# Optimization experiments

Measured on AMD Instinct MI355X. Metric: run time of the kernel, lower is better.

Reference implementation:

```python
import jax, jax.numpy as jnp
import numpy as np

N, H, E, R, Q = 10000, 128, 160000, 32, 1
CUT = 5.0  # cutoff_upper, cutoff_lower = 0


def setup_inputs() -> dict:
    key = jax.random.key(0)
    ks = jax.random.split(key, 16)

    def w(k, shape, fan_in):
        return jax.random.normal(k, shape, jnp.float32) / np.sqrt(fan_in).astype(np.float32)

    return dict(
        X=jax.random.normal(ks[0], (N, H, 3, 3), jnp.float32),
        charges=jax.random.normal(ks[1], (N, Q), jnp.float32),
        edge_attr=jax.random.normal(ks[2], (E, R), jnp.float32),
        edge_weight=jax.random.uniform(ks[3], (E,), jnp.float32, 0.0, CUT),
        W1=w(ks[4], (H, R + 2 * Q), R + 2 * Q), b1=jnp.zeros((H,), jnp.float32),
        W2=w(ks[5], (2 * H, H), H), b2=jnp.zeros((2 * H,), jnp.float32),
        W3=w(ks[6], (3 * H, 2 * H), 2 * H), b3=jnp.zeros((3 * H,), jnp.float32),
        Wt0=w(ks[7], (H, H), H), Wt1=w(ks[8], (H, H), H), Wt2=w(ks[9], (H, H), H),
        Wt3=w(ks[10], (H, H), H), Wt4=w(ks[11], (H, H), H), Wt5=w(ks[12], (H, H), H),
        edge_index=jax.random.randint(ks[13], (2, E), 0, N),
    )


def tensor_norm(T):
    return jnp.sum(T * T, axis=(-2, -1))  # [N, H]


def decompose(T):
    # I: mean of diagonal (scalar per channel); A: skew part; S: traceless symmetric part
    I = jnp.trace(T, axis1=-2, axis2=-1) / 3.0  # [N, H]
    Tt = jnp.swapaxes(T, -2, -1)
    A = 0.5 * (T - Tt)
    S = 0.5 * (T + Tt) - I[..., None, None] * jnp.eye(3, dtype=T.dtype)
    return I, A, S


def chlin(T, W):
    # channel-mixing linear on [N, H, 3, 3]; torch Linear: y_o = sum_h x_h W[o, h]
    return jnp.einsum('nhij,oh->noij', T, W)


def vec_to_skew(v):
    # v: [N, H, 3] -> skew-symmetric [N, H, 3, 3]
    z = jnp.zeros_like(v[..., 0])
    return jnp.stack([
        jnp.stack([z, -v[..., 2], v[..., 1]], -1),
        jnp.stack([v[..., 2], z, -v[..., 0]], -1),
        jnp.stack([-v[..., 1], v[..., 0], z], -1),
    ], -2)


def skew_to_vec(A):
    return jnp.stack([A[..., 2, 1], A[..., 0, 2], A[..., 1, 0]], -1)


def reference(X, charges, edge_attr, edge_weight, W1, b1, W2, b2, W3, b3,
              Wt0, Wt1, Wt2, Wt3, Wt4, Wt5, edge_index):
    eye = jnp.eye(3, dtype=X.dtype)
    src, dst = edge_index[0], edge_index[1]
    n = X.shape[0]

    # cosine cutoff (cutoff_lower = 0)
    C = 0.5 * (jnp.cos(jnp.pi * edge_weight / CUT) + 1.0) * (edge_weight < CUT)

    # edge scalar MLP
    x = jnp.concatenate([edge_attr, charges[src], charges[dst]], axis=-1)
    x = jax.nn.silu(x @ W1.T + b1)
    x = jax.nn.silu(x @ W2.T + b2)
    x = jax.nn.silu(x @ W3.T + b3)
    x = (x * C[:, None]).reshape(-1, 3, H)  # [E, 3, H]

    X = X / (tensor_norm(X) + 1.0)[..., None, None]
    I, A, S = decompose(X)
    I = I @ Wt0.T
    A = chlin(A, Wt1)
    S = chlin(S, Wt2)
    Y = A + S + I[..., None, None] * eye

    # message passing: gather at dst, weight by edge scalars, scatter-add to src
    Im = jax.ops.segment_sum(x[:, 0, :] * I[dst], src, num_segments=n)
    Am = jax.ops.segment_sum(x[:, 1, :, None] * skew_to_vec(A)[dst], src, num_segments=n)
    Sm = jax.ops.segment_sum(x[:, 2, :, None, None] * S[dst], src, num_segments=n)
    msg = vec_to_skew(Am) + Sm + Im[..., None, None] * eye

    # O(3) equivariance: symmetrized product
    M = jnp.matmul(msg, Y) + jnp.matmul(Y, msg)
    I, A, S = decompose(M)

    _X = A + S + I[..., None, None] * eye
    normp1 = tensor_norm(_X) + 1.0
    I = I / normp1
    A = A / normp1[..., None, None]
    S = S / normp1[..., None, None]
    I = I @ Wt3.T
    A = chlin(A, Wt4)
    S = chlin(S, Wt5)
    dX = A + S + I[..., None, None] * eye
    return X + dX + jnp.matmul(dX, dX)
```

## Files before the change

### kernel.cpp

```cpp
#include <hip/hip_runtime.h>

#define NN  10000
#define HD  128
#define EE  160000
#define RD  32
#define NH  (NN * HD)

typedef __attribute__((ext_vector_type(8))) short short8_t;
typedef __attribute__((ext_vector_type(4))) float f32x4_t;
typedef __attribute__((ext_vector_type(4))) int   int4_t;

__device__ __forceinline__ float silu_f(float z) {
    return z * __builtin_amdgcn_rcpf(1.0f + __expf(-z));
}
__device__ __forceinline__ short f2b(float v) {
    unsigned u = __float_as_uint(v);
    unsigned r = (u + 0x7FFFu + ((u >> 16) & 1u)) >> 16;
    return (short)r;
}
__device__ __forceinline__ float b2f(short s) {
    return __uint_as_float(((unsigned)(unsigned short)s) << 16);
}
__device__ __forceinline__ unsigned cvt_pk(float a, float b) {
    unsigned r;
    asm("v_cvt_pk_bf16_f32 %0, %1, %2" : "=v"(r) : "v"(a), "v"(b));
    return r;
}

__global__ __launch_bounds__(256) void k_wconv(
    const float* __restrict__ W1, const float* __restrict__ W2,
    const float* __restrict__ W3,
    const float* __restrict__ Wt0, const float* __restrict__ Wt1,
    const float* __restrict__ Wt2, const float* __restrict__ Wt3,
    const float* __restrict__ Wt4, const float* __restrict__ Wt5,
    short* __restrict__ W1b, short* __restrict__ W2b, short* __restrict__ W3b,
    short* __restrict__ WtPh, short* __restrict__ WtPl,
    short* __restrict__ WtFh, short* __restrict__ WtFl)
{
    const int i = blockIdx.x * 256 + threadIdx.x;
    if (i < 8192) {
        const int j = i & 7, lane = (i >> 3) & 63;
        const int kb = (i >> 9) & 1, ct = i >> 10;
        const int n = ct * 16 + (lane & 15);
        const int k = kb * 32 + (lane >> 4) * 8 + j;
        W1b[i] = (k < 34) ? f2b(W1[n * 34 + k]) : (short)0;
        return;
    }
    int j2 = i - 8192;
    if (j2 < 32768) {
        const int j = j2 & 7, lane = (j2 >> 3) & 63;
        const int kb = (j2 >> 9) & 3, ct = j2 >> 11;
        const int n = ct * 16 + (lane & 15);
        const int k = kb * 32 + (lane >> 4) * 8 + j;
        W2b[j2] = f2b(W2[n * 128 + k]);
        return;
    }
    j2 -= 32768;
    if (j2 < 98304) {
        const int j = j2 & 7, lane = (j2 >> 3) & 63;
        const int kb = (j2 >> 9) & 7, ct = j2 >> 12;
        const int n = ct * 16 + (lane & 15);
        const int k = kb * 32 + (lane >> 4) * 8 + j;
        W3b[j2] = f2b(W3[n * 256 + k]);
        return;
    }
    j2 -= 98304;
    if (j2 < 6 * 16384) {
        const int m = j2 >> 14, idx = j2 & 16383;
        const float* src = (m == 0) ? Wt0 : (m == 1) ? Wt1 : (m == 2) ? Wt2
                         : (m == 3) ? Wt3 : (m == 4) ? Wt4 : Wt5;
        const float w = src[idx];
        const short hi = f2b(w);
        const short lo = f2b(w - b2f(hi));
        if (m < 3) { WtPh[m * 16384 + idx] = hi; WtPl[m * 16384 + idx] = lo; }
        else       { WtFh[(m - 3) * 16384 + idx] = hi; WtFl[(m - 3) * 16384 + idx] = lo; }
    }
}


template <bool YBF16>
__global__ __launch_bounds__(512, 4) void k_mix_prep(
    const float* __restrict__ X,
    const short* __restrict__ Wh, const short* __restrict__ Wl,
    float* __restrict__ Yf, short* __restrict__ ybf)
{
    extern __shared__ __align__(16) char smem[];
    short* sBh = (short*)smem;
    short* sBl = sBh + 144 * 128;
    float* sC  = (float*)smem;

    const int tid = threadIdx.x;
    const int n0  = blockIdx.x * 16;

#pragma unroll 2
    for (int i = 0; i < 4; i++) {
        const int p  = i * 512 + tid;
        const int nl = p >> 7, h = p & 127;
        const float* t = X + ((size_t)((n0 + nl) * HD + h)) * 9;
        float T[9];
#pragma unroll
        for (int q = 0; q < 9; q++) T[q] = t[q];
        float nrm = 0.f;
#pragma unroll
        for (int q = 0; q < 9; q++) nrm = fmaf(T[q], T[q], nrm);
        const float inv = 1.0f / (nrm + 1.0f);
#pragma unroll
        for (int q = 0; q < 9; q++) T[q] *= inv;
        const float I = (T[0] + T[4] + T[8]) * (1.0f / 3.0f);
        float dec[9];
        dec[0] = I;
        dec[1] = 0.5f * (T[7] - T[5]);
        dec[2] = 0.5f * (T[2] - T[6]);
        dec[3] = 0.5f * (T[3] - T[1]);
        dec[4] = T[0] - I;
        dec[5] = 0.5f * (T[1] + T[3]);
        dec[6] = 0.5f * (T[2] + T[6]);
        dec[7] = T[4] - I;
        dec[8] = 0.5f * (T[5] + T[7]);
        const int sw = (nl & 7) << 3;
        const int hx = h ^ sw;
#pragma unroll
        for (int c = 0; c < 9; c++) {
            const float v  = dec[c];
            const short hi = f2b(v);
            const short lo = f2b(v - b2f(hi));
            const int idx = (c * 16 + nl) * 128 + hx;
            sBh[idx] = hi;
            sBl[idx] = lo;
        }
    }
    __syncthreads();

    const int lane = tid & 63, wid = tid >> 6;
    const int l15 = lane & 15, g = lane >> 4;
    f32x4_t acc[9];
#pragma unroll
    for (int c = 0; c < 9; c++) acc[c] = {0.f, 0.f, 0.f, 0.f};

    const int bsw = (l15 & 7) << 3;
    const int o   = wid * 16 + l15;
#pragma unroll
    for (int k = 0; k < 4; k++) {
        const int k0  = k * 32 + g * 8;
        const int ksw = k0 ^ bsw;
#pragma unroll
        for (int w = 0; w < 3; w++) {
            const size_t aoff = (size_t)w * 16384 + (size_t)o * 128 + k0;
            const short8_t Ah = *(const short8_t*)(Wh + aoff);
            const short8_t Al = *(const short8_t*)(Wl + aoff);
            const int ct0 = (w == 0) ? 0 : (w == 1 ? 1 : 4);
            const int ctn = (w == 0) ? 1 : (w == 1 ? 3 : 5);
            for (int cc = 0; cc < ctn; cc++) {
                const int ct = ct0 + cc;
                const int boff = (ct * 16 + l15) * 128 + ksw;
                const short8_t Bh = *(const short8_t*)&sBh[boff];
                const short8_t Bl = *(const short8_t*)&sBl[boff];
                acc[ct] = __builtin_amdgcn_mfma_f32_16x16x32_bf16(Al, Bh, acc[ct], 0, 0, 0);
                acc[ct] = __builtin_amdgcn_mfma_f32_16x16x32_bf16(Ah, Bl, acc[ct], 0, 0, 0);
                acc[ct] = __builtin_amdgcn_mfma_f32_16x16x32_bf16(Ah, Bh, acc[ct], 0, 0, 0);
            }
        }
    }
    __syncthreads();

    const int csw = (l15 & 7) << 2;
    {
        const int o0 = wid * 16 + g * 4;
#pragma unroll
        for (int ct = 0; ct < 9; ct++)
            *(f32x4_t*)&sC[(ct * 16 + l15) * 128 + (o0 ^ csw)] = acc[ct];
    }
    __syncthreads();

    for (int i = tid; i < 144 * 32; i += 512) {
        const int row = i >> 5, q = i & 31;
        const int c = row >> 4, nl = row & 15;
        const int sw = (nl & 7) << 2;
        const f32x4_t v = *(const f32x4_t*)&sC[row * 128 + ((q * 4) ^ sw)];
        const size_t oo = (size_t)c * NH + (size_t)(n0 + nl) * HD + q * 4;
        if constexpr (YBF16) {
            uint2 u;
            u.x = cvt_pk(v[0], v[1]);
            u.y = cvt_pk(v[2], v[3]);
            *(uint2*)&ybf[oo] = u;
        } else {
            *(f32x4_t*)&Yf[oo] = v;
        }
    }
}

template <bool FUSED>
__global__ __launch_bounds__(512, 4) void k_mix_fin(
    const float* __restrict__ X,
    const float* __restrict__ Yf,  const float* __restrict__ MSGf,
    const short* __restrict__ Ybf, const short* __restrict__ XC,
    const int* __restrict__ offs,  const int* __restrict__ DSTS,
    const short* __restrict__ Wh,  const short* __restrict__ Wl,
    float* __restrict__ outp)
{
    extern __shared__ __align__(16) char smem[];
    short* sBh = (short*)smem;
    short* sBl = sBh + 144 * 128;
    float* sC  = (float*)smem;

    const int tid = threadIdx.x;
    const int n0  = blockIdx.x * 16;

    for (int i = 0; i < 4; i++) {
        const int p  = i * 512 + tid;
        const int nl = p >> 7, h = p & 127;
        const int basep = (n0 + nl) * HD + h;
        float yv[9], mv[9];
        if constexpr (FUSED) {
            const int n = n0 + nl;
            const int beg = offs[n], end = offs[n + 1];
#pragma unroll
            for (int c = 0; c < 9; c++) mv[c] = 0.f;
            for (int pp = beg; pp < end; ++pp) {
                const int dst = DSTS[pp];
                const size_t xb = (size_t)pp * 384;
                const float x0 = b2f(XC[xb + h]);
                const float x1 = b2f(XC[xb + 128 + h]);
                const float x2 = b2f(XC[xb + 256 + h]);
                const int yb = dst * HD + h;
                mv[0] = fmaf(x0, b2f(Ybf[0 * (size_t)NH + yb]), mv[0]);
                mv[1] = fmaf(x1, b2f(Ybf[1 * (size_t)NH + yb]), mv[1]);
                mv[2] = fmaf(x1, b2f(Ybf[2 * (size_t)NH + yb]), mv[2]);
                mv[3] = fmaf(x1, b2f(Ybf[3 * (size_t)NH + yb]), mv[3]);
                mv[4] = fmaf(x2, b2f(Ybf[4 * (size_t)NH + yb]), mv[4]);
                mv[5] = fmaf(x2, b2f(Ybf[5 * (size_t)NH + yb]), mv[5]);
                mv[6] = fmaf(x2, b2f(Ybf[6 * (size_t)NH + yb]), mv[6]);
                mv[7] = fmaf(x2, b2f(Ybf[7 * (size_t)NH + yb]), mv[7]);
                mv[8] = fmaf(x2, b2f(Ybf[8 * (size_t)NH + yb]), mv[8]);
            }
#pragma unroll
            for (int c = 0; c < 9; c++) yv[c] = b2f(Ybf[(size_t)c * NH + basep]);
        } else {
#pragma unroll
            for (int c = 0; c < 9; c++) {
                yv[c] = Yf[(size_t)c * NH + basep];
                mv[c] = MSGf[(size_t)c * NH + basep];
            }
        }
        float Yt[9], G[9];
        {
            const float I = yv[0], a0 = yv[1], a1 = yv[2], a2 = yv[3];
            const float s00 = yv[4], s01 = yv[5], s02 = yv[6], s11 = yv[7], s12 = yv[8];
            const float s22 = -s00 - s11;
            Yt[0] = I + s00; Yt[1] = s01 - a2; Yt[2] = s02 + a1;
            Yt[3] = s01 + a2; Yt[4] = I + s11; Yt[5] = s12 - a0;
            Yt[6] = s02 - a1; Yt[7] = s12 + a0; Yt[8] = I + s22;
        }
        {
            const float I = mv[0], a0 = mv[1], a1 = mv[2], a2 = mv[3];
            const float s00 = mv[4], s01 = mv[5], s02 = mv[6], s11 = mv[7], s12 = mv[8];
            const float s22 = -s00 - s11;
            G[0] = I + s00; G[1] = s01 - a2; G[2] = s02 + a1;
            G[3] = s01 + a2; G[4] = I + s11; G[5] = s12 - a0;
            G[6] = s02 - a1; G[7] = s12 + a0; G[8] = I + s22;
        }
        float M[9];
#pragma unroll
        for (int r = 0; r < 3; r++)
#pragma unroll
            for (int cc = 0; cc < 3; cc++) {
                float a = 0.f;
#pragma unroll
                for (int k = 0; k < 3; k++)
                    a += G[r * 3 + k] * Yt[k * 3 + cc]
                       + Yt[r * 3 + k] * G[k * 3 + cc];
                M[r * 3 + cc] = a;
            }
        const float I2 = (M[0] + M[4] + M[8]) * (1.0f / 3.0f);
        const float a0 = 0.5f * (M[7] - M[5]);
        const float a1 = 0.5f * (M[2] - M[6]);
        const float a2 = 0.5f * (M[3] - M[1]);
        const float s00 = M[0] - I2, s11 = M[4] - I2;
        const float s01 = 0.5f * (M[1] + M[3]);
        const float s02 = 0.5f * (M[2] + M[6]);
        const float s12 = 0.5f * (M[5] + M[7]);
        const float s22 = -s00 - s11;
        const float nrm = 2.f * (a0 * a0 + a1 * a1 + a2 * a2)
                        + (s00 * s00 + s11 * s11 + s22 * s22)
                        + 2.f * (s01 * s01 + s02 * s02 + s12 * s12)
                        + 3.f * I2 * I2;
        const float inv = 1.0f / (nrm + 1.0f);
        float dec[9];
        dec[0] = I2 * inv;  dec[1] = a0 * inv;  dec[2] = a1 * inv;
        dec[3] = a2 * inv;  dec[4] = s00 * inv; dec[5] = s01 * inv;
        dec[6] = s02 * inv; dec[7] = s11 * inv; dec[8] = s12 * inv;

        const int sw = (nl & 7) << 3;
        const int hx = h ^ sw;
#pragma unroll
        for (int c = 0; c < 9; c++) {
            const float v  = dec[c];
            const short hi = f2b(v);
            const short lo = f2b(v - b2f(hi));
            const int idx = (c * 16 + nl) * 128 + hx;
            sBh[idx] = hi;
            sBl[idx] = lo;
        }
    }
    __syncthreads();

    const int lane = tid & 63, wid = tid >> 6;
    const int l15 = lane & 15, g = lane >> 4;
    f32x4_t acc[9];
#pragma unroll
    for (int c = 0; c < 9; c++) acc[c] = {0.f, 0.f, 0.f, 0.f};

    const int bsw = (l15 & 7) << 3;
    const int o   = wid * 16 + l15;
#pragma unroll
    for (int k = 0; k < 4; k++) {
        const int k0  = k * 32 + g * 8;
        const int ksw = k0 ^ bsw;
#pragma unroll
        for (int w = 0; w < 3; w++) {
            const size_t aoff = (size_t)w * 16384 + (size_t)o * 128 + k0;
            const short8_t Ah = *(const short8_t*)(Wh + aoff);
            const short8_t Al = *(const short8_t*)(Wl + aoff);
            const int ct0 = (w == 0) ? 0 : (w == 1 ? 1 : 4);
            const int ctn = (w == 0) ? 1 : (w == 1 ? 3 : 5);
            for (int cc = 0; cc < ctn; cc++) {
                const int ct = ct0 + cc;
                const int boff = (ct * 16 + l15) * 128 + ksw;
                const short8_t Bh = *(const short8_t*)&sBh[boff];
                const short8_t Bl = *(const short8_t*)&sBl[boff];
                acc[ct] = __builtin_amdgcn_mfma_f32_16x16x32_bf16(Al, Bh, acc[ct], 0, 0, 0);
                acc[ct] = __builtin_amdgcn_mfma_f32_16x16x32_bf16(Ah, Bl, acc[ct], 0, 0, 0);
                acc[ct] = __builtin_amdgcn_mfma_f32_16x16x32_bf16(Ah, Bh, acc[ct], 0, 0, 0);
            }
        }
    }
    __syncthreads();

    const int csw = (l15 & 7) << 2;
    {
        const int o0 = wid * 16 + g * 4;
#pragma unroll
        for (int ct = 0; ct < 9; ct++)
            *(f32x4_t*)&sC[(ct * 16 + l15) * 128 + (o0 ^ csw)] = acc[ct];
    }
    __syncthreads();

#pragma unroll 2
    for (int i = 0; i < 4; i++) {
        const int p  = i * 512 + tid;
        const int nl = p >> 7, oo = p & 127;
        const int sw = (nl & 7) << 2;
        const int ox = oo ^ sw;
        float a9[9];
#pragma unroll
        for (int c = 0; c < 9; c++) a9[c] = sC[(c * 16 + nl) * 128 + ox];
        float D[9];
        {
            const float I = a9[0], a0 = a9[1], a1 = a9[2], a2 = a9[3];
            const float s00 = a9[4], s01 = a9[5], s02 = a9[6];
            const float s11 = a9[7], s12 = a9[8];
            const float s22 = -s00 - s11;
            D[0] = I + s00; D[1] = s01 - a2; D[2] = s02 + a1;
            D[3] = s01 + a2; D[4] = I + s11; D[5] = s12 - a0;
            D[6] = s02 - a1; D[7] = s12 + a0; D[8] = I + s22;
        }
        const size_t xbase = ((size_t)((n0 + nl) * HD + oo)) * 9;
        float T[9];
#pragma unroll
        for (int q = 0; q < 9; q++) T[q] = X[xbase + q];
        float nrm = 0.f;
#pragma unroll
        for (int q = 0; q < 9; q++) nrm = fmaf(T[q], T[q], nrm);
        const float inv = 1.0f / (nrm + 1.0f);
        float* op = outp + xbase;
#pragma unroll
        for (int r = 0; r < 3; r++)
#pragma unroll
            for (int cc = 0; cc < 3; cc++) {
                float dd2 = 0.f;
#pragma unroll
                for (int k = 0; k < 3; k++)
                    dd2 = fmaf(D[r * 3 + k], D[k * 3 + cc], dd2);
                op[r * 3 + cc] = T[r * 3 + cc] * inv + D[r * 3 + cc] + dd2;
            }
    }
}

__global__ __launch_bounds__(256) void k_count(const int* __restrict__ EI,
                                               int* __restrict__ cnt)
{
    const int e = blockIdx.x * 256 + threadIdx.x;
    atomicAdd(&cnt[EI[e]], 1);
}

__global__ __launch_bounds__(256) void k_scan(const int* __restrict__ cnt,
                                              int* __restrict__ offs,
                                              int* __restrict__ cur)
{
    __shared__ int part[256];
    const int tid = threadIdx.x;
    const int per = (NN + 255) / 256;
    int s = 0;
    for (int i = 0; i < per; i++) {
        const int idx = tid * per + i;
        if (idx < NN) s += cnt[idx];
    }
    part[tid] = s;
    __syncthreads();
    if (tid == 0) {
        int r = 0;
        for (int i = 0; i < 256; i++) { const int t = part[i]; part[i] = r; r += t; }
        offs[NN] = r;
    }
    __syncthreads();
    int run = part[tid];
    for (int i = 0; i < per; i++) {
        const int idx = tid * per + i;
        if (idx < NN) {
            offs[idx] = run;
            cur[idx]  = run;
            run += cnt[idx];
        }
    }
}

__global__ __launch_bounds__(256) void k_fill(const int* __restrict__ EI,
                                              int* __restrict__ cur,
                                              int* __restrict__ EIDS,
                                              int* __restrict__ DSTS)
{
    const int e = blockIdx.x * 256 + threadIdx.x;
    const int s = EI[e];
    const int pos = atomicAdd(&cur[s], 1);
    EIDS[pos] = e;
    DSTS[pos] = EI[EE + e];
}

__global__ __launch_bounds__(512, 4) void k_edge_mfma(
    const float* __restrict__ EA, const float* __restrict__ CH,
    const float* __restrict__ EW, const int*   __restrict__ EI,
    const int*   __restrict__ EIDS,
    const short* __restrict__ W1b, const float* __restrict__ b1,
    const short* __restrict__ W2b, const float* __restrict__ b2,
    const short* __restrict__ W3b, const float* __restrict__ b3,
    short* __restrict__ XC)
{
    __shared__ __align__(16) short sH2[64 * 256];
    __shared__ __align__(16) short sH1[64 * 128];
    __shared__ float sCut[64];
    __shared__ int   sEid[64];

    short* sIn = sH2;
    const int tid = threadIdx.x;
    const int e0  = blockIdx.x * 64;

    {
        int4_t z = {0, 0, 0, 0};
        ((int4_t*)sIn)[tid] = z;
        if (tid < 64) sEid[tid] = EIDS[e0 + tid];
    }
    __syncthreads();
    {
        const int ee  = tid >> 3;
        const int eid = sEid[ee];
        const float4 v = *(const float4*)(EA + (size_t)eid * RD + (tid & 7) * 4);
        const int k = (tid & 7) * 4;
        short4 sv;
        sv.x = f2b(v.x); sv.y = f2b(v.y); sv.z = f2b(v.z); sv.w = f2b(v.w);
        *(short4*)&sIn[ee * 64 + (k ^ ((ee & 7) << 3))] = sv;
        if (tid < 64) {
            const int e2  = tid;
            const int eid2 = sEid[e2];
            const int s = EI[eid2];
            const int d = EI[EE + eid2];
            const int sw = (e2 & 7) << 3;
            sIn[e2 * 64 + (32 ^ sw)] = f2b(CH[s]);
            sIn[e2 * 64 + (33 ^ sw)] = f2b(CH[d]);
            const float w = EW[eid2];
            sCut[e2] = (w < 5.0f)
                     ? 0.5f * (__cosf(0.62831853071795864769f * w) + 1.0f) : 0.0f;
        }
    }
    __syncthreads();

    const int lane = tid & 63;
    const int wid  = tid >> 6;
    const int l15  = lane & 15;
    const int g    = lane >> 4;
    const int fsw  = l15 << 3;

    {
        short8_t E1[4][2];
#pragma unroll
        for (int at = 0; at < 4; at++) {
            const int row = at * 16 + l15;
            const int x = (row & 7) << 3;
            E1[at][0] = *(const short8_t*)&sIn[row * 64 + ((g * 8) ^ x)];
            E1[at][1] = *(const short8_t*)&sIn[row * 64 + ((32 + g * 8) ^ x)];
        }
        const int ct = wid;
        const float4 b4 = *(const float4*)&b1[ct * 16 + g * 4];
        const short8_t av0 = *(const short8_t*)(W1b + (size_t)((ct * 2 + 0) * 64 + lane) * 8);
        const short8_t av1 = *(const short8_t*)(W1b + (size_t)((ct * 2 + 1) * 64 + lane) * 8);
        const int fcol = ct * 16 + g * 4;
#pragma unroll
        for (int at = 0; at < 4; at++) {
            f32x4_t acc = {b4.x, b4.y, b4.z, b4.w};
            acc = __builtin_amdgcn_mfma_f32_16x16x32_bf16(av0, E1[at][0], acc, 0, 0, 0);
            acc = __builtin_amdgcn_mfma_f32_16x16x32_bf16(av1, E1[at][1], acc, 0, 0, 0);
            const int edge = at * 16 + l15;
            uint2 u;
            u.x = cvt_pk(silu_f(acc[0]), silu_f(acc[1]));
            u.y = cvt_pk(silu_f(acc[2]), silu_f(acc[3]));
            *(uint2*)&sH1[edge * 128 + (fcol ^ fsw)] = u;
        }
    }
    __syncthreads();

    {
        short8_t E2[4][4];
#pragma unroll
        for (int at = 0; at < 4; at++) {
            const int row = at * 16 + l15;
            const int x = (row & 15) << 3;
#pragma unroll
            for (int kb = 0; kb < 4; kb++)
                E2[at][kb] = *(const short8_t*)&sH1[row * 128 + ((kb * 32 + g * 8) ^ x)];
        }
#pragma unroll
        for (int c = 0; c < 2; c++) {
            const int ct = c * 8 + wid;
            const float4 b4 = *(const float4*)&b2[ct * 16 + g * 4];
            const int fcol = ct * 16 + g * 4;
            f32x4_t acc[4];
#pragma unroll
            for (int at = 0; at < 4; at++) acc[at] = {b4.x, b4.y, b4.z, b4.w};
#pragma unroll
            for (int kb = 0; kb < 4; kb++) {
                const short8_t av = *(const short8_t*)(W2b + (size_t)((ct * 4 + kb) * 64 + lane) * 8);
#pragma unroll
                for (int at = 0; at < 4; at++)
                    acc[at] = __builtin_amdgcn_mfma_f32_16x16x32_bf16(av, E2[at][kb], acc[at], 0, 0, 0);
            }
#pragma unroll
            for (int at = 0; at < 4; at++) {
                const int edge = at * 16 + l15;
                uint2 u;
                u.x = cvt_pk(silu_f(acc[at][0]), silu_f(acc[at][1]));
                u.y = cvt_pk(silu_f(acc[at][2]), silu_f(acc[at][3]));
                *(uint2*)&sH2[edge * 256 + (fcol ^ fsw)] = u;
            }
        }
    }
    __syncthreads();

    {
        short8_t E3[4][8];
#pragma unroll
        for (int at = 0; at < 4; at++) {
            const int row = at * 16 + l15;
            const int x = (row & 15) << 3;
#pragma unroll
            for (int kb = 0; kb < 8; kb++)
                E3[at][kb] = *(const short8_t*)&sH2[row * 256 + ((kb * 32 + g * 8) ^ x)];
        }
        float cut[4];
#pragma unroll
        for (int at = 0; at < 4; at++) cut[at] = sCut[at * 16 + l15];
        for (int c = 0; c < 3; c++) {
            const int ct = c * 8 + wid;
            const float4 b4 = *(const float4*)&b3[ct * 16 + g * 4];
            const int fcol = ct * 16 + g * 4;
            f32x4_t acc[4];
#pragma unroll
            for (int at = 0; at < 4; at++) acc[at] = {b4.x, b4.y, b4.z, b4.w};
#pragma unroll
            for (int kb = 0; kb < 8; kb++) {
                const short8_t av = *(const short8_t*)(W3b + (size_t)((ct * 8 + kb) * 64 + lane) * 8);
#pragma unroll
                for (int at = 0; at < 4; at++)
                    acc[at] = __builtin_amdgcn_mfma_f32_16x16x32_bf16(av, E3[at][kb], acc[at], 0, 0, 0);
            }
#pragma unroll
            for (int at = 0; at < 4; at++) {
                const int edge = at * 16 + l15;
                const float cv = cut[at];
                uint2 u;
                u.x = cvt_pk(silu_f(acc[at][0]) * cv, silu_f(acc[at][1]) * cv);
                u.y = cvt_pk(silu_f(acc[at][2]) * cv, silu_f(acc[at][3]) * cv);
                *(uint2*)&XC[(size_t)(e0 + edge) * 384 + fcol] = u;
            }
        }
    }
}

__global__ __launch_bounds__(256) void k_edge_atomic(
    const float* __restrict__ EA, const float* __restrict__ CH,
    const float* __restrict__ EW, const int*   __restrict__ EI,
    const float* __restrict__ W1, const float* __restrict__ b1,
    const float* __restrict__ W2, const float* __restrict__ b2,
    const float* __restrict__ W3, const float* __restrict__ b3,
    const float* __restrict__ Y,  float* __restrict__ MSG)
{
    __shared__ __align__(16) float sInf[32 * 35];
    __shared__ __align__(16) float sH1f[32 * 132];
    __shared__ __align__(16) float sH2f[32 * 260];
    __shared__ __align__(16) float sXcf[32 * 132];
    __shared__ float sCc[32];
    __shared__ int   sS[32], sD[32];

    const int e0  = blockIdx.x * 32;
    const int tid = threadIdx.x;

    {
        const float4 v = ((const float4*)(EA + (size_t)e0 * RD))[tid];
        const int e = tid >> 3;
        const int k = (tid & 7) * 4;
        float* p = sInf + e * 35 + k;
        p[0] = v.x; p[1] = v.y; p[2] = v.z; p[3] = v.w;
    }
    if (tid < 32) {
        const int e = tid;
        const int s = EI[e0 + e];
        const int d = EI[EE + e0 + e];
        sS[e] = s; sD[e] = d;
        sInf[e * 35 + 32] = CH[s];
        sInf[e * 35 + 33] = CH[d];
        const float w = EW[e0 + e];
        sCc[e] = (w < 5.0f) ? 0.5f * (__cosf(0.62831853071795864769f * w) + 1.0f)
                            : 0.0f;
    }
    __syncthreads();

    const int e  = tid & 31;
    const int og = tid >> 5;

    {
        float acc[16];
#pragma unroll
        for (int j = 0; j < 16; j++) acc[j] = b1[og * 16 + j];
        for (int k = 0; k < 34; k++) {
            const float v = sInf[e * 35 + k];
#pragma unroll
            for (int j = 0; j < 16; j++)
                acc[j] = fmaf(v, W1[(og * 16 + j) * 34 + k], acc[j]);
        }
#pragma unroll
        for (int j = 0; j < 16; j++)
            sH1f[e * 132 + og * 16 + j] = silu_f(acc[j]);
    }
    __syncthreads();

    {
        float acc[32];
#pragma unroll
        for (int j = 0; j < 32; j++) acc[j] = b2[og * 32 + j];
        for (int hq = 0; hq < 32; hq++) {
            const float4 v = *(const float4*)&sH1f[e * 132 + hq * 4];
#pragma unroll
            for (int j = 0; j < 32; j++) {
                const float4 w =
                    *(const float4*)&W2[(size_t)(og * 32 + j) * 128 + hq * 4];
                acc[j] = fmaf(v.x, w.x, fmaf(v.y, w.y,
                         fmaf(v.z, w.z, fmaf(v.w, w.w, acc[j]))));
            }
        }
#pragma unroll
        for (int j = 0; j < 32; j++)
            sH2f[e * 260 + og * 32 + j] = silu_f(acc[j]);
    }
    __syncthreads();

    for (int c = 0; c < 3; c++) {
        {
            float acc[16];
#pragma unroll
            for (int j = 0; j < 16; j++) acc[j] = b3[c * 128 + og * 16 + j];
            for (int hq = 0; hq < 64; hq++) {
                const float4 v = *(const float4*)&sH2f[e * 260 + hq * 4];
#pragma unroll
                for (int j = 0; j < 16; j++) {
                    const float4 w = *(const float4*)
                        &W3[(size_t)(c * 128 + og * 16 + j) * 256 + hq * 4];
                    acc[j] = fmaf(v.x, w.x, fmaf(v.y, w.y,
                             fmaf(v.z, w.z, fmaf(v.w, w.w, acc[j]))));
                }
            }
            const float cc = sCc[e];
#pragma unroll
            for (int j = 0; j < 16; j++)
                sXcf[e * 132 + og * 16 + j] = silu_f(acc[j]) * cc;
        }
        __syncthreads();
        {
            const int h  = tid & 127;
            const int eh = tid >> 7;
#pragma unroll 4
            for (int i = 0; i < 16; i++) {
                const int ee = (eh << 4) | i;
                const int s = sS[ee], d = sD[ee];
                const float xv = sXcf[ee * 132 + h];
                const int sb = s * HD + h, db = d * HD + h;
                if (c == 0) {
                    atomicAdd(&MSG[0 * (size_t)NH + sb], xv * Y[0 * (size_t)NH + db]);
                } else if (c == 1) {
#pragma unroll
                    for (int cc2 = 1; cc2 < 4; cc2++)
                        atomicAdd(&MSG[(size_t)cc2 * NH + sb],
                                  xv * Y[(size_t)cc2 * NH + db]);
                } else {
#pragma unroll
                    for (int cc2 = 4; cc2 < 9; cc2++)
                        atomicAdd(&MSG[(size_t)cc2 * NH + sb],
                                  xv * Y[(size_t)cc2 * NH + db]);
                }
            }
        }
        __syncthreads();
    }
}

static inline size_t align_up(size_t v, size_t a) { return (v + a - 1) & ~(a - 1); }

extern "C" void kernel_launch(void* const* d_in, const int* in_sizes, int n_in,
                              void* d_out, int out_size, void* d_ws, size_t ws_size,
                              hipStream_t stream)
{
    const float* X   = (const float*)d_in[0];
    const float* CH  = (const float*)d_in[1];
    const float* EA  = (const float*)d_in[2];
    const float* EW  = (const float*)d_in[3];
    const float* W1  = (const float*)d_in[4];
    const float* b1  = (const float*)d_in[5];
    const float* W2  = (const float*)d_in[6];
    const float* b2  = (const float*)d_in[7];
    const float* W3  = (const float*)d_in[8];
    const float* b3  = (const float*)d_in[9];
    const float* Wt0 = (const float*)d_in[10];
    const float* Wt1 = (const float*)d_in[11];
    const float* Wt2 = (const float*)d_in[12];
    const float* Wt3 = (const float*)d_in[13];
    const float* Wt4 = (const float*)d_in[14];
    const float* Wt5 = (const float*)d_in[15];
    const int*   EI  = (const int*)d_in[16];
    float* out = (float*)d_out;

    size_t off = 0;
    float* Y    = (float*)((char*)d_ws + off); off = align_up(off + (size_t)9 * NH * 4, 64);
    float* MSG  = (float*)((char*)d_ws + off); off = align_up(off + (size_t)9 * NH * 4, 64);
    int*   cnt  = (int*)((char*)d_ws + off);   off = align_up(off + (size_t)NN * 4, 64);
    int*   cur  = (int*)((char*)d_ws + off);   off = align_up(off + (size_t)NN * 4, 64);
    int*   offs = (int*)((char*)d_ws + off);   off = align_up(off + (size_t)(NN + 1) * 4, 64);
    int*   EIDS = (int*)((char*)d_ws + off);   off = align_up(off + (size_t)EE * 4, 64);
    int*   DSTS = (int*)((char*)d_ws + off);   off = align_up(off + (size_t)EE * 4, 64);
    short* W1b  = (short*)((char*)d_ws + off); off = align_up(off + (size_t)8192 * 2, 64);
    short* W2b  = (short*)((char*)d_ws + off); off = align_up(off + (size_t)32768 * 2, 64);
    short* W3b  = (short*)((char*)d_ws + off); off = align_up(off + (size_t)98304 * 2, 64);
    short* WtPh = (short*)((char*)d_ws + off); off = align_up(off + (size_t)3 * 16384 * 2, 64);
    short* WtPl = (short*)((char*)d_ws + off); off = align_up(off + (size_t)3 * 16384 * 2, 64);
    short* WtFh = (short*)((char*)d_ws + off); off = align_up(off + (size_t)3 * 16384 * 2, 64);
    short* WtFl = (short*)((char*)d_ws + off); off = align_up(off + (size_t)3 * 16384 * 2, 64);
    short* XC   = (short*)((char*)d_ws + off); off = align_up(off + (size_t)EE * 384 * 2, 64);
    short* Ybf  = (short*)((char*)d_ws + off); off = align_up(off + (size_t)9 * NH * 2, 64);
    const size_t need_fast = off;

    k_wconv<<<928, 256, 0, stream>>>(W1, W2, W3, Wt0, Wt1, Wt2, Wt3, Wt4, Wt5,
                                     W1b, W2b, W3b, WtPh, WtPl, WtFh, WtFl);

    if (ws_size >= need_fast) {
        k_mix_prep<true><<<NN / 16, 512, 73728, stream>>>(X, WtPh, WtPl, Y, Ybf);

        hipMemsetAsync(cnt, 0, (size_t)NN * sizeof(int), stream);
        k_count<<<EE / 256, 256, 0, stream>>>(EI, cnt);
        k_scan<<<1, 256, 0, stream>>>(cnt, offs, cur);
        k_fill<<<EE / 256, 256, 0, stream>>>(EI, cur, EIDS, DSTS);
        k_edge_mfma<<<EE / 64, 512, 0, stream>>>(EA, CH, EW, EI, EIDS,
                                                 W1b, b1, W2b, b2, W3b, b3, XC);
        k_mix_fin<true><<<NN / 16, 512, 73728, stream>>>(
            X, Y, MSG, Ybf, XC, offs, DSTS, WtFh, WtFl, out);
    } else {
        k_mix_prep<false><<<NN / 16, 512, 73728, stream>>>(X, WtPh, WtPl, Y, Ybf);
        hipMemsetAsync(MSG, 0, (size_t)9 * NH * sizeof(float), stream);
        k_edge_atomic<<<EE / 32, 256, 0, stream>>>(EA, CH, EW, EI,
                                                   W1, b1, W2, b2, W3, b3, Y, MSG);
        k_mix_fin<false><<<NN / 16, 512, 73728, stream>>>(
            X, Y, MSG, Ybf, XC, offs, DSTS, WtFh, WtFl, out);
    }
}
```

Baseline: 346.9 us.

## Split CSR gather out of mix_fin into a separate small-block kernel

```diff
diff --git a/kernel.cpp b/kernel.cpp
--- a/kernel.cpp
+++ b/kernel.cpp
@@ -26,6 +26,8 @@
     asm("v_cvt_pk_bf16_f32 %0, %1, %2" : "=v"(r) : "v"(a), "v"(b));
     return r;
 }
+__device__ __forceinline__ float ldy(const float* p) { return *p; }
+__device__ __forceinline__ float ldy(const short* p) { return b2f(*p); }
 
 __global__ __launch_bounds__(256) void k_wconv(
     const float* __restrict__ W1, const float* __restrict__ W2,
@@ -76,7 +78,6 @@
         else       { WtFh[(m - 3) * 16384 + idx] = hi; WtFl[(m - 3) * 16384 + idx] = lo; }
     }
 }
-
 
 template <bool YBF16>
 __global__ __launch_bounds__(512, 4) void k_mix_prep(
@@ -189,13 +190,11 @@
     }
 }
 
-template <bool FUSED>
+template <typename YT, typename MT>
 __global__ __launch_bounds__(512, 4) void k_mix_fin(
     const float* __restrict__ X,
-    const float* __restrict__ Yf,  const float* __restrict__ MSGf,
-    const short* __restrict__ Ybf, const short* __restrict__ XC,
-    const int* __restrict__ offs,  const int* __restrict__ DSTS,
-    const short* __restrict__ Wh,  const short* __restrict__ Wl,
+    const YT* __restrict__ Yp, const MT* __restrict__ Mp,
+    const short* __restrict__ Wh, const short* __restrict__ Wl,
     float* __restrict__ outp)
 {
     extern __shared__ __align__(16) char smem[];
@@ -206,41 +205,16 @@
     const int tid = threadIdx.x;
     const int n0  = blockIdx.x * 16;
 
+#pragma unroll 2
     for (int i = 0; i < 4; i++) {
         const int p  = i * 512 + tid;
         const int nl = p >> 7, h = p & 127;
         const int basep = (n0 + nl) * HD + h;
         float yv[9], mv[9];
-        if constexpr (FUSED) {
-            const int n = n0 + nl;
-            const int beg = offs[n], end = offs[n + 1];
-#pragma unroll
-            for (int c = 0; c < 9; c++) mv[c] = 0.f;
-            for (int pp = beg; pp < end; ++pp) {
-                const int dst = DSTS[pp];
-                const size_t xb = (size_t)pp * 384;
-                const float x0 = b2f(XC[xb + h]);
-                const float x1 = b2f(XC[xb + 128 + h]);
-                const float x2 = b2f(XC[xb + 256 + h]);
-                const int yb = dst * HD + h;
-                mv[0] = fmaf(x0, b2f(Ybf[0 * (size_t)NH + yb]), mv[0]);
-                mv[1] = fmaf(x1, b2f(Ybf[1 * (size_t)NH + yb]), mv[1]);
-                mv[2] = fmaf(x1, b2f(Ybf[2 * (size_t)NH + yb]), mv[2]);
-                mv[3] = fmaf(x1, b2f(Ybf[3 * (size_t)NH + yb]), mv[3]);
-                mv[4] = fmaf(x2, b2f(Ybf[4 * (size_t)NH + yb]), mv[4]);
-                mv[5] = fmaf(x2, b2f(Ybf[5 * (size_t)NH + yb]), mv[5]);
-                mv[6] = fmaf(x2, b2f(Ybf[6 * (size_t)NH + yb]), mv[6]);
-                mv[7] = fmaf(x2, b2f(Ybf[7 * (size_t)NH + yb]), mv[7]);
-                mv[8] = fmaf(x2, b2f(Ybf[8 * (size_t)NH + yb]), mv[8]);
-            }
-#pragma unroll
-            for (int c = 0; c < 9; c++) yv[c] = b2f(Ybf[(size_t)c * NH + basep]);
-        } else {
-#pragma unroll
-            for (int c = 0; c < 9; c++) {
-                yv[c] = Yf[(size_t)c * NH + basep];
-                mv[c] = MSGf[(size_t)c * NH + basep];
-            }
+#pragma unroll
+        for (int c = 0; c < 9; c++) {
+            yv[c] = ldy(Yp + (size_t)c * NH + basep);
+            mv[c] = ldy(Mp + (size_t)c * NH + basep);
         }
         float Yt[9], G[9];
         {
@@ -594,6 +568,42 @@
     }
 }
 
+__global__ __launch_bounds__(256) void k_gather(
+    const short* __restrict__ XC, const short* __restrict__ Y,
+    const int* __restrict__ offs, const int* __restrict__ DSTS,
+    short* __restrict__ MSGb)
+{
+    const int tid = threadIdx.x;
+    const int nl  = tid >> 7, h = tid & 127;
+    const int n   = blockIdx.x * 2 + nl;
+    const int beg = offs[n], end = offs[n + 1];
+
+    float m[9];
+#pragma unroll
+    for (int c = 0; c < 9; c++) m[c] = 0.f;
+
+    for (int p = beg; p < end; ++p) {
+        const int dst = DSTS[p];
+        const size_t xb = (size_t)p * 384;
+        const float x0 = b2f(XC[xb + h]);
+        const float x1 = b2f(XC[xb + 128 + h]);
+        const float x2 = b2f(XC[xb + 256 + h]);
+        const int yb = dst * HD + h;
+        m[0] = fmaf(x0, b2f(Y[0 * (size_t)NH + yb]), m[0]);
+        m[1] = fmaf(x1, b2f(Y[1 * (size_t)NH + yb]), m[1]);
+        m[2] = fmaf(x1, b2f(Y[2 * (size_t)NH + yb]), m[2]);
+        m[3] = fmaf(x1, b2f(Y[3 * (size_t)NH + yb]), m[3]);
+        m[4] = fmaf(x2, b2f(Y[4 * (size_t)NH + yb]), m[4]);
+        m[5] = fmaf(x2, b2f(Y[5 * (size_t)NH + yb]), m[5]);
+        m[6] = fmaf(x2, b2f(Y[6 * (size_t)NH + yb]), m[6]);
+        m[7] = fmaf(x2, b2f(Y[7 * (size_t)NH + yb]), m[7]);
+        m[8] = fmaf(x2, b2f(Y[8 * (size_t)NH + yb]), m[8]);
+    }
+    const int base = n * HD + h;
+#pragma unroll
+    for (int c = 0; c < 9; c++) MSGb[(size_t)c * NH + base] = f2b(m[c]);
+}
+
 __global__ __launch_bounds__(256) void k_edge_atomic(
     const float* __restrict__ EA, const float* __restrict__ CH,
     const float* __restrict__ EW, const int*   __restrict__ EI,
@@ -748,6 +758,7 @@
     size_t off = 0;
     float* Y    = (float*)((char*)d_ws + off); off = align_up(off + (size_t)9 * NH * 4, 64);
     float* MSG  = (float*)((char*)d_ws + off); off = align_up(off + (size_t)9 * NH * 4, 64);
+    short* MSGb = (short*)MSG;
     int*   cnt  = (int*)((char*)d_ws + off);   off = align_up(off + (size_t)NN * 4, 64);
     int*   cur  = (int*)((char*)d_ws + off);   off = align_up(off + (size_t)NN * 4, 64);
     int*   offs = (int*)((char*)d_ws + off);   off = align_up(off + (size_t)(NN + 1) * 4, 64);
@@ -776,14 +787,15 @@
         k_fill<<<EE / 256, 256, 0, stream>>>(EI, cur, EIDS, DSTS);
         k_edge_mfma<<<EE / 64, 512, 0, stream>>>(EA, CH, EW, EI, EIDS,
                                                  W1b, b1, W2b, b2, W3b, b3, XC);
-        k_mix_fin<true><<<NN / 16, 512, 73728, stream>>>(
-            X, Y, MSG, Ybf, XC, offs, DSTS, WtFh, WtFl, out);
+        k_gather<<<NN / 2, 256, 0, stream>>>(XC, Ybf, offs, DSTS, MSGb);
+        k_mix_fin<short, short><<<NN / 16, 512, 73728, stream>>>(
+            X, Ybf, MSGb, WtFh, WtFl, out);
     } else {
         k_mix_prep<false><<<NN / 16, 512, 73728, stream>>>(X, WtPh, WtPl, Y, Ybf);
         hipMemsetAsync(MSG, 0, (size_t)9 * NH * sizeof(float), stream);
         k_edge_atomic<<<EE / 32, 256, 0, stream>>>(EA, CH, EW, EI,
                                                    W1, b1, W2, b2, W3, b3, Y, MSG);
-        k_mix_fin<false><<<NN / 16, 512, 73728, stream>>>(
-            X, Y, MSG, Ybf, XC, offs, DSTS, WtFh, WtFl, out);
-    }
-}
+        k_mix_fin<float, float><<<NN / 16, 512, 73728, stream>>>(
+            X, Y, MSG, WtFh, WtFl, out);
+    }
+}
```

New measurement: 295.8 us. -14.7%, faster.
